# Performance work log

Measured on AMD Instinct MI355X. Metric: run time of the kernel, lower is better.

## Reference

```python
import jax, jax.numpy as jnp
import numpy as np

B, T, D, E, FF, K = 4, 1024, 1024, 8, 2048, 2
SINKHORN_ITERS = 3


def setup_inputs() -> dict:
    key = jax.random.key(0)
    ks = jax.random.split(key, 7)
    scale = 0.02
    return {
        "x": jax.random.normal(ks[0], (B, T, D), dtype=jnp.float32),
        "router_w": jax.random.normal(ks[1], (E, D), dtype=jnp.float32) * scale,  # nn.Linear(D,E).weight
        "router_b": jnp.zeros((E,), dtype=jnp.float32),
        "temperature": jnp.ones((1,), dtype=jnp.float32) * 0.5,
        "wg": jax.random.normal(ks[2], (E, D, FF), dtype=jnp.float32) * scale,   # expert gate weights
        "wp": jax.random.normal(ks[3], (E, D, FF), dtype=jnp.float32) * scale,   # expert proj weights
        "wo": jax.random.normal(ks[4], (E, FF, D), dtype=jnp.float32) * scale,   # expert out_proj weights
    }


def _sinkhorn(log_alpha, iters=SINKHORN_ITERS):
    for _ in range(iters):
        log_alpha = log_alpha - jax.nn.logsumexp(log_alpha, axis=-1, keepdims=True)
        log_alpha = log_alpha - jax.nn.logsumexp(log_alpha, axis=-2, keepdims=True)
    gates = jnp.exp(log_alpha)
    return gates / (jnp.sum(gates, axis=-1, keepdims=True) + 1e-8)


def reference(x, router_w, router_b, temperature, wg, wp, wo):
    # Router scores with clamped temperature (clamp(min=0.1))
    temp = jnp.maximum(temperature, 0.1)
    scores = (jnp.einsum("btd,ed->bte", x, router_w) + router_b) / temp  # [B,T,E]

    # T>1 and E>1 -> Sinkhorn doubly-stochastic normalization
    gates = _sinkhorn(scores)

    topk_vals, topk_idx = jax.lax.top_k(gates, K)                 # [B,T,K]
    topk_gates = topk_vals / (jnp.sum(topk_vals, axis=-1, keepdims=True) + 1e-8)

    # Dense all-expert FFN (relu-gated GLU), matching mask-and-sum semantics.
    # sum_k sum_i (idx_k==i)*gate_k*expert_i(x) == sum_k gate_k * expert_{idx_k}(x)
    g = jax.nn.relu(jnp.einsum("btd,edf->btef", x, wg))           # [B,T,E,FF]
    p = jnp.einsum("btd,edf->btef", x, wp)                        # [B,T,E,FF]
    all_out = jnp.einsum("btef,efd->bted", g * p, wo)             # [B,T,E,D]

    gathered = jnp.take_along_axis(all_out, topk_idx[..., None], axis=2)  # [B,T,K,D]
    expert_out = jnp.sum(gathered * topk_gates[..., None], axis=2)        # [B,T,D]

    return x + expert_out
```

## Files before the change

### kernel.cpp

```cpp
#include <hip/hip_runtime.h>
#include <hip/hip_bf16.h>
#include <stdint.h>

#define B_   4
#define T_   1024
#define D_   1024
#define E_   8
#define FF_  2048
#define NT_  4096
#define LCAP 9472
#define NTS1 (D_ / 64)
#define NT2  (FF_ / 32)

typedef unsigned short u16;
typedef __attribute__((ext_vector_type(8))) short bf16x8;
typedef __attribute__((ext_vector_type(4))) float f32x4;

#define MFMA16(a, b, c) __builtin_amdgcn_mfma_f32_16x16x32_bf16((a), (b), (c), 0, 0, 0)

__device__ __forceinline__ u16 f2bf(float f) {
  union { float f; uint32_t u; } c; c.f = f;
  return (u16)((c.u + 0x7FFFu + ((c.u >> 16) & 1u)) >> 16);
}

__device__ __forceinline__ void gl_lds16(const void* g, void* l) {
  __builtin_amdgcn_global_load_lds(
      (const __attribute__((address_space(1))) uint32_t*)g,
      (__attribute__((address_space(3))) uint32_t*)l, 16, 0, 0);
}


__global__ __launch_bounds__(256) void k_router(const float* __restrict__ x,
                                                const float* __restrict__ rw,
                                                const float* __restrict__ rb,
                                                const float* __restrict__ temp,
                                                float* __restrict__ scores,
                                                float* __restrict__ out,
                                                u16* __restrict__ xb,
                                                int* __restrict__ tok, float* __restrict__ gate,
                                                int* __restrict__ cnt, int* __restrict__ cur) {
  const int gid = blockIdx.x * 256 + threadIdx.x;
  if (gid < LCAP) { tok[gid] = 0; gate[gid] = 0.f; }
  if (gid < E_)   { cnt[gid] = 0; cur[gid] = 0; }

  int wid  = gid >> 6;
  int lane = threadIdx.x & 63;
  const float* xr = x + (size_t)wid * D_;
  float* orow = out + (size_t)wid * D_;
  u16* xrow = xb + (size_t)wid * D_;
  float acc[E_];
  #pragma unroll
  for (int e = 0; e < E_; ++e) acc[e] = 0.f;
  for (int i = lane; i < D_; i += 64) {
    float xv = xr[i];
    orow[i] = xv;
    xrow[i] = f2bf(xv);
    #pragma unroll
    for (int e = 0; e < E_; ++e) acc[e] += xv * rw[e * D_ + i];
  }
  float inv = 1.0f / fmaxf(temp[0], 0.1f);
  #pragma unroll
  for (int e = 0; e < E_; ++e) {
    float v = acc[e];
    for (int off = 32; off; off >>= 1) v += __shfl_xor(v, off);
    if (lane == 0) scores[(size_t)wid * E_ + e] = (v + rb[e]) * inv;
  }
}

__global__ __launch_bounds__(1024) void k_sinkhorn(const float* __restrict__ scores,
                                                   float* __restrict__ tkg, int* __restrict__ tki,
                                                   int* __restrict__ cnt) {
  const int b = blockIdx.x, t = threadIdx.x;
  const int row = b * T_ + t;
  float s[E_];
  #pragma unroll
  for (int e = 0; e < E_; ++e) s[e] = scores[(size_t)row * E_ + e];

  __shared__ float red[16][E_];
  __shared__ float redv[E_];
  __shared__ int lcnt[E_];
  if (t < E_) lcnt[t] = 0;
  const int wid = t >> 6, lane = t & 63;

  for (int it = 0; it < 3; ++it) {
    float m = s[0];
    #pragma unroll
    for (int e = 1; e < E_; ++e) m = fmaxf(m, s[e]);
    float sum = 0.f;
    #pragma unroll
    for (int e = 0; e < E_; ++e) sum += expf(s[e] - m);
    float lse = m + logf(sum);
    #pragma unroll
    for (int e = 0; e < E_; ++e) s[e] -= lse;

    #pragma unroll
    for (int e = 0; e < E_; ++e) {
      float v = s[e];
      for (int off = 32; off; off >>= 1) v = fmaxf(v, __shfl_xor(v, off));
      if (lane == 0) red[wid][e] = v;
    }
    __syncthreads();
    if (t < E_) {
      float mm = red[0][t];
      #pragma unroll
      for (int wv = 1; wv < 16; ++wv) mm = fmaxf(mm, red[wv][t]);
      redv[t] = mm;
    }
    __syncthreads();
    float cm[E_];
    #pragma unroll
    for (int e = 0; e < E_; ++e) cm[e] = redv[e];

    #pragma unroll
    for (int e = 0; e < E_; ++e) {
      float v = expf(s[e] - cm[e]);
      for (int off = 32; off; off >>= 1) v += __shfl_xor(v, off);
      if (lane == 0) red[wid][e] = v;
    }
    __syncthreads();
    if (t < E_) {
      float ss = 0.f;
      #pragma unroll
      for (int wv = 0; wv < 16; ++wv) ss += red[wv][t];
      redv[t] = ss;
    }
    __syncthreads();
    #pragma unroll
    for (int e = 0; e < E_; ++e) s[e] -= cm[e] + logf(redv[e]);
    __syncthreads();
  }

  float g[E_]; float rs = 0.f;
  #pragma unroll
  for (int e = 0; e < E_; ++e) { g[e] = expf(s[e]); rs += g[e]; }
  float inv = 1.f / (rs + 1e-8f);
  #pragma unroll
  for (int e = 0; e < E_; ++e) g[e] *= inv;

  int i0 = 0; float v0 = g[0];
  #pragma unroll
  for (int e = 1; e < E_; ++e) if (g[e] > v0) { v0 = g[e]; i0 = e; }
  int i1 = -1; float v1 = -1e30f;
  #pragma unroll
  for (int e = 0; e < E_; ++e) if (e != i0 && g[e] > v1) { v1 = g[e]; i1 = e; }
  float den = 1.f / (v0 + v1 + 1e-8f);
  tkg[row * 2 + 0] = v0 * den; tki[row * 2 + 0] = i0;
  tkg[row * 2 + 1] = v1 * den; tki[row * 2 + 1] = i1;

  atomicAdd(&lcnt[i0], 1);
  atomicAdd(&lcnt[i1], 1);
  __syncthreads();
  if (t < E_) atomicAdd(&cnt[t], lcnt[t]);
}

__global__ void k_offsets(const int* __restrict__ cnt, int* __restrict__ segoff) {
  if (threadIdx.x == 0 && blockIdx.x == 0) {
    int run = 0;
    for (int e = 0; e < E_; ++e) { segoff[e] = run; run += ((cnt[e] + 127) >> 7) << 7; }
    segoff[E_] = run;
  }
}

__global__ __launch_bounds__(256) void k_scatter(const int* __restrict__ tki, const float* __restrict__ tkg,
                                                 const int* __restrict__ segoff, int* __restrict__ cur,
                                                 int* __restrict__ tok, float* __restrict__ gate) {
  int idx = blockIdx.x * 256 + threadIdx.x;
  int row = idx >> 1;
  int e = tki[idx];
  float g = tkg[idx];
  int pos = atomicAdd(&cur[e], 1);
  int p = segoff[e] + pos;
  tok[p] = row;
  gate[p] = g;
}


__global__ __launch_bounds__(256) void k_transpose_wgp(const float* __restrict__ wg,
                                                       const float* __restrict__ wp,
                                                       u16* __restrict__ wa) {
  __shared__ __align__(16) u16 ldsT[128][136];
  const int e = blockIdx.z >> 1, iswp = blockIdx.z & 1;
  const float* src = (iswp ? wp : wg) + (size_t)e * D_ * FF_;
  const int woff = iswp * 16;
  const int f0 = blockIdx.x * 128, d0 = blockIdx.y * 128;
  const int tid = threadIdx.x;
  #pragma unroll
  for (int it = 0; it < 16; ++it) {
    const int fi = it * 256 + tid;
    const int rowd = fi >> 5;
    const int col4 = fi & 31;
    const float4 v = *(const float4*)(src + (size_t)(d0 + rowd) * FF_ + f0 + col4 * 4);
    ldsT[col4 * 4 + 0][rowd] = f2bf(v.x);
    ldsT[col4 * 4 + 1][rowd] = f2bf(v.y);
    ldsT[col4 * 4 + 2][rowd] = f2bf(v.z);
    ldsT[col4 * 4 + 3][rowd] = f2bf(v.w);
  }
  __syncthreads();
  const int cl = tid >> 1, half = tid & 1;
  const int f = f0 + cl;
  const int fp = ((f >> 4) << 5) + (f & 15) + woff;
  u16* dst = wa + (size_t)e * 4096 * 1024 + (size_t)fp * 1024 + d0 + half * 64;
  const u16* srcl = &ldsT[cl][half * 64];
  #pragma unroll
  for (int i = 0; i < 8; ++i)
    *(uint4*)(dst + i * 8) = *(const uint4*)(srcl + i * 8);
}

__global__ __launch_bounds__(256) void k_transpose_wo(const float* __restrict__ wo,
                                                      u16* __restrict__ woT) {
  __shared__ __align__(16) u16 ldsT[128][136];
  const int e = blockIdx.z;
  const float* src = wo + (size_t)e * FF_ * D_;
  const int d0 = blockIdx.x * 128, ff0 = blockIdx.y * 128;
  const int tid = threadIdx.x;
  #pragma unroll
  for (int it = 0; it < 16; ++it) {
    const int fi = it * 256 + tid;
    const int rowf = fi >> 5;
    const int col4 = fi & 31;
    const float4 v = *(const float4*)(src + (size_t)(ff0 + rowf) * D_ + d0 + col4 * 4);
    ldsT[col4 * 4 + 0][rowf] = f2bf(v.x);
    ldsT[col4 * 4 + 1][rowf] = f2bf(v.y);
    ldsT[col4 * 4 + 2][rowf] = f2bf(v.z);
    ldsT[col4 * 4 + 3][rowf] = f2bf(v.w);
  }
  __syncthreads();
  const int dl = tid >> 1, half = tid & 1;
  u16* dst = woT + (size_t)e * D_ * FF_ + (size_t)(d0 + dl) * FF_ + ff0 + half * 64;
  const u16* srcl = &ldsT[dl][half * 64];
  #pragma unroll
  for (int i = 0; i < 8; ++i)
    *(uint4*)(dst + i * 8) = *(const uint4*)(srcl + i * 8);
}


__global__ __launch_bounds__(512, 2) void k_stage1(
    const u16* __restrict__ wa, const u16* __restrict__ xb,
    const int* __restrict__ tok, const int* __restrict__ segoff,
    u16* __restrict__ H) {
  const int raw = blockIdx.x;
  const int e   = raw & 7;
  const int rem = raw >> 3;
  const int ft  = rem >> 4;
  const int pt2 = rem & 15;
  const int seg0 = segoff[e], segend = segoff[e + 1];
  if (pt2 * 256 >= segend - seg0) return;
  const int tid = threadIdx.x;
  const int lane = tid & 63;
  const int w = tid >> 6;
  const int lane15 = lane & 15, lchunk = lane >> 4;
  const int lk8 = lchunk * 8;
  const int fw = w >> 2, pw = w & 3;

  __shared__ __align__(16) u16 LA[2][16384];
  __shared__ __align__(16) u16 LB[2][16384];

  const int prow0 = seg0 + pt2 * 256;
  const u16* asrc0 = wa + (size_t)e * 4096 * 1024
                        + (size_t)(ft * 256 + 2 * w * 16 + lane15) * 1024 + lk8;
  const u16* asrc1 = asrc0 + 16 * 1024;
  const int tk0 = tok[prow0 + 2 * w * 16 + lane15];
  const int tk1 = tok[prow0 + 2 * w * 16 + 16 + lane15];
  const u16* bsrc0 = xb + (size_t)tk0 * D_ + lk8;
  const u16* bsrc1 = xb + (size_t)tk1 * D_ + lk8;
  const int dA0 = 2 * w * 512, dA1 = dA0 + 512;

  const f32x4 vz = {0.f, 0.f, 0.f, 0.f};
  f32x4 acc[8][4];
  #pragma unroll
  for (int m = 0; m < 8; ++m)
    #pragma unroll
    for (int n = 0; n < 4; ++n) acc[m][n] = vz;

#define STG_A(c, s) do { const int o_ = (s) * 64;           \
    gl_lds16(asrc0 + o_,      &LA[c][dA0]);                 \
    gl_lds16(asrc0 + o_ + 32, &LA[c][dA0 + 8192]);          \
    gl_lds16(asrc1 + o_,      &LA[c][dA1]);                 \
    gl_lds16(asrc1 + o_ + 32, &LA[c][dA1 + 8192]); } while (0)
#define STG_B(c, s) do { const int o_ = (s) * 64;           \
    gl_lds16(bsrc0 + o_,      &LB[c][dA0]);                 \
    gl_lds16(bsrc0 + o_ + 32, &LB[c][dA0 + 8192]);          \
    gl_lds16(bsrc1 + o_,      &LB[c][dA1]);                 \
    gl_lds16(bsrc1 + o_ + 32, &LB[c][dA1 + 8192]); } while (0)

  STG_A(0, 0); STG_B(0, 0);
  #pragma unroll 1
  for (int s = 0; s < NTS1; ++s) {
    const int c = s & 1;
    asm volatile("s_waitcnt vmcnt(0)" ::: "memory");
    __builtin_amdgcn_s_barrier();
    asm volatile("" ::: "memory");
    const u16* la = LA[c];
    const u16* lb = LB[c];
    bf16x8 bv[4][2];
    #pragma unroll
    for (int n = 0; n < 4; ++n)
      #pragma unroll
      for (int kc = 0; kc < 2; ++kc)
        bv[n][kc] = *(const bf16x8*)(lb + kc * 8192 + (pw * 4 + n) * 512 + lane * 8);
    #pragma unroll
    for (int p = 0; p < 4; ++p) {
      bf16x8 av[2][2];
      #pragma unroll
      for (int mm = 0; mm < 2; ++mm)
        #pragma unroll
        for (int kc = 0; kc < 2; ++kc)
          av[mm][kc] = *(const bf16x8*)(la + kc * 8192 + (fw * 8 + 2 * p + mm) * 512 + lane * 8);
      if (p == 0) { if (s + 1 < NTS1) STG_A(c ^ 1, s + 1); }
      if (p == 1) { if (s + 1 < NTS1) STG_B(c ^ 1, s + 1); }
      __builtin_amdgcn_s_setprio(1);
      #pragma unroll
      for (int mm = 0; mm < 2; ++mm)
        #pragma unroll
        for (int n = 0; n < 4; ++n)
          #pragma unroll
          for (int kc = 0; kc < 2; ++kc)
            acc[2 * p + mm][n] = MFMA16(av[mm][kc], bv[n][kc], acc[2 * p + mm][n]);
      __builtin_amdgcn_s_setprio(0);
      if (p < 3) {
        __builtin_amdgcn_s_barrier();
        asm volatile("" ::: "memory");
      }
    }
  }
#undef STG_A
#undef STG_B

  const int jrow = lchunk * 4;
  #pragma unroll
  for (int q = 0; q < 4; ++q) {
    const int fcol = ft * 128 + fw * 64 + q * 16 + jrow;
    #pragma unroll
    for (int n = 0; n < 4; ++n) {
      const int prow = prow0 + pw * 64 + n * 16 + lane15;
      if (prow < segend) {
        union { uint2 v; u16 s[4]; } u;
        #pragma unroll
        for (int j = 0; j < 4; ++j)
          u.s[j] = f2bf(fmaxf(acc[2 * q][n][j], 0.f) * acc[2 * q + 1][n][j]);
        *(uint2*)(H + (size_t)prow * FF_ + fcol) = u.v;
      }
    }
  }
}

__global__ __launch_bounds__(512, 4) void k_stage2(
    const u16* __restrict__ H, const u16* __restrict__ woT,
    const int* __restrict__ tok, const float* __restrict__ gate,
    const int* __restrict__ cnt, const int* __restrict__ segoff,
    float* __restrict__ out) {
  const int raw = blockIdx.x;
  const int e   = raw & 7;
  const int rem = raw >> 3;
  const int dt  = rem >> 5;
  const int pt  = rem & 31;
  if (pt * 128 >= cnt[e]) return;
  const int tid = threadIdx.x;
  const int lane = tid & 63;
  const int w = tid >> 6;
  const int lane15 = lane & 15, lchunk = lane >> 4;
  const int ph = w >> 2, dq = w & 3;

  __shared__ __align__(16) u16 LH[3][4096];
  __shared__ __align__(16) u16 LW[3][4096];
  __shared__ int   ltok[128];
  __shared__ float lgt[128];

  const int prow0 = segoff[e] + pt * 128;
  if (tid < 128) { ltok[tid] = tok[prow0 + tid]; lgt[tid] = gate[prow0 + tid]; }

  const u16* hsrc = H + (size_t)(prow0 + w * 16 + lane15) * FF_ + lchunk * 8;
  const u16* wsrc = woT + (size_t)e * D_ * FF_
                        + (size_t)(dt * 128 + w * 16 + lane15) * FF_ + lchunk * 8;
  const int dstb = w * 512;

  const f32x4 vz = {0.f, 0.f, 0.f, 0.f};
  f32x4 acc[4][2];
  #pragma unroll
  for (int m = 0; m < 4; ++m)
    #pragma unroll
    for (int n = 0; n < 2; ++n) acc[m][n] = vz;

#define ISSUE2(c, t) do { const int o_ = (t) * 32;                 \
    gl_lds16(hsrc + o_, &LH[c][dstb]);                             \
    gl_lds16(wsrc + o_, &LW[c][dstb]); } while (0)

#define COMP2(c) do {                                                        \
    const u16* lh = LH[c]; const u16* lw = LW[c];                            \
    bf16x8 ah[4], bw[2];                                                     \
    _Pragma("unroll")                                                        \
    for (int m = 0; m < 4; ++m)                                              \
      ah[m] = *(const bf16x8*)(lh + (ph * 4 + m) * 512 + lane * 8);          \
    _Pragma("unroll")                                                        \
    for (int n = 0; n < 2; ++n)                                              \
      bw[n] = *(const bf16x8*)(lw + (dq * 2 + n) * 512 + lane * 8);          \
    __builtin_amdgcn_s_setprio(1);                                           \
    _Pragma("unroll")                                                        \
    for (int m = 0; m < 4; ++m)                                              \
      _Pragma("unroll")                                                      \
      for (int n = 0; n < 2; ++n)                                            \
        acc[m][n] = MFMA16(ah[m], bw[n], acc[m][n]);                         \
    __builtin_amdgcn_s_setprio(0); } while (0)

  ISSUE2(0, 0);
  ISSUE2(1, 1);
  #pragma unroll 1
  for (int t = 0; t < NT2 - 1; ++t) {
    asm volatile("s_waitcnt vmcnt(2)" ::: "memory");
    __builtin_amdgcn_s_barrier();
    asm volatile("" ::: "memory");
    if (t + 2 < NT2) { const int cn = (t + 2) % 3; ISSUE2(cn, t + 2); }
    const int c = t % 3;
    COMP2(c);
  }
  asm volatile("s_waitcnt vmcnt(0)" ::: "memory");
  __builtin_amdgcn_s_barrier();
  asm volatile("" ::: "memory");
  COMP2((NT2 - 1) % 3);
#undef ISSUE2
#undef COMP2

  const int jrow = lchunk * 4;
  #pragma unroll
  for (int m = 0; m < 4; ++m) {
    #pragma unroll
    for (int n = 0; n < 2; ++n) {
      const int dcol = dt * 128 + dq * 32 + n * 16 + lane15;
      #pragma unroll
      for (int j = 0; j < 4; ++j) {
        const int pl = ph * 64 + m * 16 + jrow + j;
        unsafeAtomicAdd(&out[(size_t)ltok[pl] * D_ + dcol], lgt[pl] * acc[m][n][j]);
      }
    }
  }
}


extern "C" void kernel_launch(void* const* d_in, const int* in_sizes, int n_in,
                              void* d_out, int out_size, void* d_ws, size_t ws_size,
                              hipStream_t stream) {
  const float* x    = (const float*)d_in[0];
  const float* rw   = (const float*)d_in[1];
  const float* rb   = (const float*)d_in[2];
  const float* temp = (const float*)d_in[3];
  const float* wg   = (const float*)d_in[4];
  const float* wp   = (const float*)d_in[5];
  const float* wo   = (const float*)d_in[6];
  float* out = (float*)d_out;
  char* ws = (char*)d_ws;

  const size_t O_XB  = 0;
  const size_t O_WA  = 8388608;
  const size_t O_WOT = O_WA;
  const size_t O_H   = O_WA + 67108864;
  const size_t O_SC  = O_H + (size_t)LCAP * FF_ * 2;
  const size_t O_TKG = O_SC + (size_t)NT_ * E_ * 4;
  const size_t O_TKI = O_TKG + (size_t)NT_ * 2 * 4;
  const size_t O_CNT = O_TKI + (size_t)NT_ * 2 * 4;
  const size_t O_CUR = O_CNT + 128;
  const size_t O_SEG = O_CUR + 128;
  const size_t O_TOK = O_SEG + 128;
  const size_t O_GTE = O_TOK + (size_t)LCAP * 4;
  const size_t REQ   = O_GTE + (size_t)LCAP * 4;
  if (ws_size < REQ) return;

  u16*   xb     = (u16*)(ws + O_XB);
  u16*   wa     = (u16*)(ws + O_WA);
  u16*   woT    = (u16*)(ws + O_WOT);
  u16*   Hbuf   = (u16*)(ws + O_H);
  float* scores = (float*)(ws + O_SC);
  float* tkg    = (float*)(ws + O_TKG);
  int*   tki    = (int*)(ws + O_TKI);
  int*   cnt    = (int*)(ws + O_CNT);
  int*   cur    = (int*)(ws + O_CUR);
  int*   segoff = (int*)(ws + O_SEG);
  int*   tok    = (int*)(ws + O_TOK);
  float* gate   = (float*)(ws + O_GTE);

  k_router<<<NT_ / 4, 256, 0, stream>>>(x, rw, rb, temp, scores, out, xb,
                                        tok, gate, cnt, cur);
  k_sinkhorn<<<B_, 1024, 0, stream>>>(scores, tkg, tki, cnt);
  k_offsets<<<1, 64, 0, stream>>>(cnt, segoff);
  k_scatter<<<(NT_ * 2) / 256, 256, 0, stream>>>(tki, tkg, segoff, cur, tok, gate);

  k_transpose_wgp<<<dim3(FF_ / 128, D_ / 128, E_ * 2), 256, 0, stream>>>(wg, wp, wa);

  k_stage1<<<16 * 16 * E_, 512, 0, stream>>>(wa, xb, tok, segoff, Hbuf);

  k_transpose_wo<<<dim3(D_ / 128, FF_ / 128, E_), 256, 0, stream>>>(wo, woT);

  k_stage2<<<32 * 8 * E_, 512, 0, stream>>>(Hbuf, woT, tok, gate, cnt, segoff, out);
}
```

Measured before the change: 463.3 us.

## Restructure stage2 pipeline to double-buffered 64-wide K steps with split staging

The stage-2 down-projection GEMM now uses K steps of 64 instead of 32, double-buffered in LDS instead of triple-buffered with 32-wide steps. The next tile's H and W loads are issued separately between two compute halves, with a mid-iteration barrier so the H buffer can be refilled while the rest of the MFMAs run. This halves the number of barrier-synchronized iterations and gives each step more MFMA work. LDS use grows and occupancy drops (launch bounds 4 to 2). The wait before each iteration is now vmcnt(0), so prefetch depth is only one step.

```diff
diff --git a/kernel.cpp b/kernel.cpp
--- a/kernel.cpp
+++ b/kernel.cpp
@@ -10,7 +10,7 @@
 #define NT_  4096
 #define LCAP 9472
 #define NTS1 (D_ / 64)
-#define NT2  (FF_ / 32)
+#define NTS2 (FF_ / 64)
 
 typedef unsigned short u16;
 typedef __attribute__((ext_vector_type(8))) short bf16x8;
@@ -344,7 +344,7 @@
   }
 }
 
-__global__ __launch_bounds__(512, 4) void k_stage2(
+__global__ __launch_bounds__(512, 2) void k_stage2(
     const u16* __restrict__ H, const u16* __restrict__ woT,
     const int* __restrict__ tok, const float* __restrict__ gate,
     const int* __restrict__ cnt, const int* __restrict__ segoff,
@@ -359,19 +359,20 @@
   const int lane = tid & 63;
   const int w = tid >> 6;
   const int lane15 = lane & 15, lchunk = lane >> 4;
+  const int lk8 = lchunk * 8;
   const int ph = w >> 2, dq = w & 3;
 
-  __shared__ __align__(16) u16 LH[3][4096];
-  __shared__ __align__(16) u16 LW[3][4096];
+  __shared__ __align__(16) u16 LH[2][8192];
+  __shared__ __align__(16) u16 LW[2][8192];
   __shared__ int   ltok[128];
   __shared__ float lgt[128];
 
   const int prow0 = segoff[e] + pt * 128;
   if (tid < 128) { ltok[tid] = tok[prow0 + tid]; lgt[tid] = gate[prow0 + tid]; }
 
-  const u16* hsrc = H + (size_t)(prow0 + w * 16 + lane15) * FF_ + lchunk * 8;
+  const u16* hsrc = H + (size_t)(prow0 + w * 16 + lane15) * FF_ + lk8;
   const u16* wsrc = woT + (size_t)e * D_ * FF_
-                        + (size_t)(dt * 128 + w * 16 + lane15) * FF_ + lchunk * 8;
+                        + (size_t)(dt * 128 + w * 16 + lane15) * FF_ + lk8;
   const int dstb = w * 512;
 
   const f32x4 vz = {0.f, 0.f, 0.f, 0.f};
@@ -381,44 +382,55 @@
     #pragma unroll
     for (int n = 0; n < 2; ++n) acc[m][n] = vz;
 
-#define ISSUE2(c, t) do { const int o_ = (t) * 32;                 \
-    gl_lds16(hsrc + o_, &LH[c][dstb]);                             \
-    gl_lds16(wsrc + o_, &LW[c][dstb]); } while (0)
-
-#define COMP2(c) do {                                                        \
-    const u16* lh = LH[c]; const u16* lw = LW[c];                            \
-    bf16x8 ah[4], bw[2];                                                     \
-    _Pragma("unroll")                                                        \
-    for (int m = 0; m < 4; ++m)                                              \
-      ah[m] = *(const bf16x8*)(lh + (ph * 4 + m) * 512 + lane * 8);          \
-    _Pragma("unroll")                                                        \
-    for (int n = 0; n < 2; ++n)                                              \
-      bw[n] = *(const bf16x8*)(lw + (dq * 2 + n) * 512 + lane * 8);          \
-    __builtin_amdgcn_s_setprio(1);                                           \
-    _Pragma("unroll")                                                        \
-    for (int m = 0; m < 4; ++m)                                              \
-      _Pragma("unroll")                                                      \
-      for (int n = 0; n < 2; ++n)                                            \
-        acc[m][n] = MFMA16(ah[m], bw[n], acc[m][n]);                         \
-    __builtin_amdgcn_s_setprio(0); } while (0)
-
-  ISSUE2(0, 0);
-  ISSUE2(1, 1);
+#define STG_H(c, s) do { const int o_ = (s) * 64;           \
+    gl_lds16(hsrc + o_,      &LH[c][dstb]);                 \
+    gl_lds16(hsrc + o_ + 32, &LH[c][dstb + 4096]); } while (0)
+#define STG_W(c, s) do { const int o_ = (s) * 64;           \
+    gl_lds16(wsrc + o_,      &LW[c][dstb]);                 \
+    gl_lds16(wsrc + o_ + 32, &LW[c][dstb + 4096]); } while (0)
+
+  STG_H(0, 0); STG_W(0, 0);
   #pragma unroll 1
-  for (int t = 0; t < NT2 - 1; ++t) {
-    asm volatile("s_waitcnt vmcnt(2)" ::: "memory");
+  for (int s = 0; s < NTS2; ++s) {
+    const int c = s & 1;
+    asm volatile("s_waitcnt vmcnt(0)" ::: "memory");
     __builtin_amdgcn_s_barrier();
     asm volatile("" ::: "memory");
-    if (t + 2 < NT2) { const int cn = (t + 2) % 3; ISSUE2(cn, t + 2); }
-    const int c = t % 3;
-    COMP2(c);
-  }
-  asm volatile("s_waitcnt vmcnt(0)" ::: "memory");
-  __builtin_amdgcn_s_barrier();
-  asm volatile("" ::: "memory");
-  COMP2((NT2 - 1) % 3);
-#undef ISSUE2
-#undef COMP2
+    const u16* lh = LH[c];
+    const u16* lw = LW[c];
+    bf16x8 bw[2][2];
+    #pragma unroll
+    for (int n = 0; n < 2; ++n)
+      #pragma unroll
+      for (int kc = 0; kc < 2; ++kc)
+        bw[n][kc] = *(const bf16x8*)(lw + kc * 4096 + (dq * 2 + n) * 512 + lane * 8);
+    #pragma unroll
+    for (int p = 0; p < 2; ++p) {
+      bf16x8 ah[2][2];
+      #pragma unroll
+      for (int mm = 0; mm < 2; ++mm)
+        #pragma unroll
+        for (int kc = 0; kc < 2; ++kc)
+          ah[mm][kc] = *(const bf16x8*)(lh + kc * 4096 + (ph * 4 + 2 * p + mm) * 512 + lane * 8);
+      if (p == 0) { if (s + 1 < NTS2) STG_H(c ^ 1, s + 1); }
+      if (p == 1) { if (s + 1 < NTS2) STG_W(c ^ 1, s + 1); }
+      __builtin_amdgcn_s_setprio(1);
+      #pragma unroll
+      for (int mm = 0; mm < 2; ++mm)
+        #pragma unroll
+        for (int n = 0; n < 2; ++n)
+          #pragma unroll
+          for (int kc = 0; kc < 2; ++kc)
+            acc[2 * p + mm][n] = MFMA16(ah[mm][kc], bw[n][kc], acc[2 * p + mm][n]);
+      __builtin_amdgcn_s_setprio(0);
+      if (p == 0) {
+        __builtin_amdgcn_s_barrier();
+        asm volatile("" ::: "memory");
+      }
+    }
+  }
+#undef STG_H
+#undef STG_W
 
   const int jrow = lchunk * 4;
   #pragma unroll
```

After: 465.8 us. No clear change (+0.5%).
